# Performance work log

Measured on AMD Instinct MI355X. Metric: run time of the kernel, lower is better.

Reference implementation:

```python
import jax, jax.numpy as jnp
import numpy as np

B = 64            # number of graphs
N = 2048          # nodes per graph (equal segments; torch.stack in the original requires this)
D = 256           # hidden_dim
G = 4             # num_groups
SUBS = 3          # subclasses per group -> num_classes = 12
C = G * SUBS


def _layer_norm(x, g, b, eps=1e-5):
    mu = jnp.mean(x, axis=-1, keepdims=True)
    var = jnp.var(x, axis=-1, keepdims=True)
    return (x - mu) * jax.lax.rsqrt(var + eps) * g + b


def setup_inputs() -> dict:
    key = jax.random.key(0)
    ks = jax.random.split(key, 20)
    T = B * N
    inp = {
        "node_features": jax.random.normal(ks[0], (T, D), dtype=jnp.float32),
        "batch": jnp.repeat(jnp.arange(B, dtype=jnp.int64), N),  # sorted, equal-size segments
        # group queries (nn.Parameter randn)
        "group_queries": jax.random.normal(ks[1], (G, D), dtype=jnp.float32),
        # per-group projector MLP: D -> 2D -> SUBS*D (stacked over groups)
        "proj_w1": jax.random.normal(ks[2], (G, D, 2 * D), dtype=jnp.float32) * (1.0 / np.sqrt(D)),
        "proj_b1": jnp.zeros((G, 2 * D), dtype=jnp.float32),
        "proj_w2": jax.random.normal(ks[3], (G, 2 * D, SUBS * D), dtype=jnp.float32) * (1.0 / np.sqrt(2 * D)),
        "proj_b2": jnp.zeros((G, SUBS * D), dtype=jnp.float32),
        # output_proj_12: LN -> Linear(D, D//2) -> ReLU -> Linear(D//2, 1)
        "ln12_g": jnp.ones((D,), dtype=jnp.float32),
        "ln12_b": jnp.zeros((D,), dtype=jnp.float32),
        "w12a": jax.random.normal(ks[4], (D, D // 2), dtype=jnp.float32) * (1.0 / np.sqrt(D)),
        "b12a": jnp.zeros((D // 2,), dtype=jnp.float32),
        "w12b": jax.random.normal(ks[5], (D // 2, 1), dtype=jnp.float32) * (1.0 / np.sqrt(D // 2)),
        "b12b": jnp.zeros((1,), dtype=jnp.float32),
        # output_proj_4
        "ln4_g": jnp.ones((D,), dtype=jnp.float32),
        "ln4_b": jnp.zeros((D,), dtype=jnp.float32),
        "w4a": jax.random.normal(ks[6], (D, D // 2), dtype=jnp.float32) * (1.0 / np.sqrt(D)),
        "b4a": jnp.zeros((D // 2,), dtype=jnp.float32),
        "w4b": jax.random.normal(ks[7], (D // 2, 1), dtype=jnp.float32) * (1.0 / np.sqrt(D // 2)),
        "b4b": jnp.zeros((1,), dtype=jnp.float32),
    }
    return inp


def reference(node_features, batch, group_queries, proj_w1, proj_b1, proj_w2, proj_b2,
              ln12_g, ln12_b, w12a, b12a, w12b, b12b,
              ln4_g, ln4_b, w4a, b4a, w4b, b4b):
    # --- derive class queries from group queries (per-group MLP) ---
    h = jax.nn.relu(jnp.einsum('gd,gdh->gh', group_queries, proj_w1) + proj_b1)   # [G, 2D]
    flat = jnp.einsum('gh,ghk->gk', h, proj_w2) + proj_b2                         # [G, SUBS*D]
    # group g maps to global class indices [3g, 3g+1, 3g+2] -> simple reshape gives ordered queries
    class_queries = flat.reshape(C, D)                                            # [12, D]

    scale = jnp.asarray(D ** 0.5, node_features.dtype)
    # equal-size sorted segments: reshape total nodes into [B, N, D] per-graph blocks
    nodes = node_features.reshape(B, N, D)

    # --- 12-class attention pooling ---
    scores12 = jnp.einsum('cd,bnd->bcn', class_queries, nodes) / scale            # [B, 12, N]
    attn12 = jax.nn.softmax(scores12, axis=-1)
    pooled12 = jnp.einsum('bcn,bnd->bcd', attn12, nodes)                          # [B, 12, D]
    x12 = _layer_norm(pooled12, ln12_g, ln12_b)
    logits_12 = (jax.nn.relu(x12 @ w12a + b12a) @ w12b + b12b)[..., 0]            # [B, 12]

    # --- 4-group attention pooling ---
    scores4 = jnp.einsum('gd,bnd->bgn', group_queries, nodes) / scale             # [B, 4, N]
    attn4 = jax.nn.softmax(scores4, axis=-1)
    pooled4 = jnp.einsum('bgn,bnd->bgd', attn4, nodes)                            # [B, 4, D]
    x4 = _layer_norm(pooled4, ln4_g, ln4_b)
    logits_4 = (jax.nn.relu(x4 @ w4a + b4a) @ w4b + b4b)[..., 0]                  # [B, 4]

    return (logits_12, logits_4, attn12)
```

## Files before the change

### kernel.cpp

```cpp
#include <hip/hip_runtime.h>
#include <math.h>

#define BG   64
#define NN   2048
#define DD   256
#define CQ   16
#define CS   128
#define NCH  16

static constexpr size_t WS_Q16 = 0;
static constexpr size_t WS_H   = 4096;
static constexpr size_t WS_S   = 6144;
static constexpr size_t WS_ML  = WS_S + (size_t)BG * 12 * NN;
static constexpr size_t WS_PL  = WS_ML + (size_t)BG * NCH * 32;

__global__ __launch_bounds__(256) void kA1(const float* __restrict__ gq,
                                           const float* __restrict__ w1,
                                           const float* __restrict__ b1,
                                           float* __restrict__ ws) {
    int blk = blockIdx.x;
    int g   = blk >> 4;
    int jb  = (blk & 15) * 32;
    int t   = threadIdx.x;
    __shared__ float qlds[256];
    qlds[t] = gq[g * 256 + t];
    if ((blk & 15) == 0) ws[WS_Q16 + (12 + g) * 256 + t] = gq[g * 256 + t];
    __syncthreads();
    int jl = t & 31, dp = t >> 5;
    float acc = 0.f;
    const float* wp = w1 + ((size_t)g * 256) * 512 + jb + jl;
    #pragma unroll 8
    for (int i = 0; i < 32; ++i) {
        int d = dp * 32 + i;
        acc += qlds[d] * wp[(size_t)d * 512];
    }
    __shared__ float red[8][33];
    red[dp][jl] = acc;
    __syncthreads();
    if (dp == 0) {
        float s = 0.f;
        #pragma unroll
        for (int p = 0; p < 8; ++p) s += red[p][jl];
        s += b1[g * 512 + jb + jl];
        ws[WS_H + g * 512 + jb + jl] = fmaxf(s, 0.f);
    }
}

__global__ __launch_bounds__(256) void kA2(const float* __restrict__ w2,
                                           const float* __restrict__ b2,
                                           float* __restrict__ ws) {
    int blk = blockIdx.x;
    int g   = blk / 48;
    int kb  = (blk % 48) * 16;
    int t   = threadIdx.x;
    __shared__ float hlds[512];
    hlds[t]       = ws[WS_H + g * 512 + t];
    hlds[t + 256] = ws[WS_H + g * 512 + t + 256];
    __syncthreads();
    int kl = t & 15, dp = t >> 4;
    float acc = 0.f;
    const float* wp = w2 + ((size_t)g * 512) * 768 + kb + kl;
    #pragma unroll 8
    for (int i = 0; i < 32; ++i) {
        int jj = dp * 32 + i;
        acc += hlds[jj] * wp[(size_t)jj * 768];
    }
    __shared__ float red[16][17];
    red[dp][kl] = acc;
    __syncthreads();
    if (dp == 0) {
        float s = 0.f;
        #pragma unroll
        for (int p = 0; p < 16; ++p) s += red[p][kl];
        ws[WS_Q16 + g * 768 + kb + kl] = s + b2[g * 768 + kb + kl];
    }
}

__global__ __launch_bounds__(256, 4) void kF(const float* __restrict__ x,
                                             float* __restrict__ ws) {
    __shared__ float4 qlds[CQ * 64];
    __shared__ float  wlds[CQ * CS];
    __shared__ float  mbuf[CQ], lbuf[CQ];

    int t   = threadIdx.x;
    int blk = blockIdx.x;
    int b   = blk >> 4, ch = blk & 15;
    int gn0 = b * NN + ch * CS;

    const float4* qg = (const float4*)(ws + WS_Q16);
    #pragma unroll
    for (int i = 0; i < 4; ++i) qlds[t + i * 256] = qg[t + i * 256];
    __syncthreads();

    int node = t & 127, half = t >> 7;
    const float4* xa = (const float4*)x + (size_t)(gn0 + node) * 64 + half * 32;
    float sc[CQ];
    #pragma unroll
    for (int c = 0; c < CQ; ++c) sc[c] = 0.f;

    float4 buf[8];
    #pragma unroll
    for (int i = 0; i < 8; ++i) buf[i] = xa[i];
    for (int base = 0; base < 32; base += 8) {
        float4 cur[8];
        #pragma unroll
        for (int i = 0; i < 8; ++i) cur[i] = buf[i];
        if (base + 8 < 32) {
            #pragma unroll
            for (int i = 0; i < 8; ++i) buf[i] = xa[base + 8 + i];
        }
        #pragma unroll
        for (int i = 0; i < 8; ++i) {
            #pragma unroll
            for (int c = 0; c < CQ; ++c) {
                float4 q = qlds[c * 64 + half * 32 + base + i];
                sc[c] += q.x * cur[i].x + q.y * cur[i].y
                       + q.z * cur[i].z + q.w * cur[i].w;
            }
        }
    }

    if (half == 1) {
        #pragma unroll
        for (int c = 0; c < CQ; ++c) wlds[c * CS + node] = sc[c];
    }
    __syncthreads();
    if (half == 0) {
        #pragma unroll
        for (int c = 0; c < CQ; ++c)
            wlds[c * CS + node] = (sc[c] + wlds[c * CS + node]) * 0.0625f;
    }
    __syncthreads();

    {
        float* srow = ws + WS_S + (size_t)b * 12 * NN + ch * CS;
        #pragma unroll
        for (int k = 0; k < 6; ++k) {
            int idx = k * 256 + t;
            srow[(size_t)(idx >> 7) * NN + (idx & 127)] = wlds[idx];
        }
    }

    {
        int c = t >> 4, slot = t & 15;
        float mv = -1e30f;
        #pragma unroll
        for (int k = 0; k < 8; ++k) mv = fmaxf(mv, wlds[c * CS + slot + k * 16]);
        #pragma unroll
        for (int off = 1; off < 16; off <<= 1) mv = fmaxf(mv, __shfl_xor(mv, off, 64));
        if (slot == 0) mbuf[c] = mv;
    }
    __syncthreads();
    #pragma unroll
    for (int k = 0; k < 8; ++k) {
        int idx = k * 256 + t;
        wlds[idx] = __expf(wlds[idx] - mbuf[idx >> 7]);
    }
    __syncthreads();
    {
        int c = t >> 4, slot = t & 15;
        float lv = 0.f;
        #pragma unroll
        for (int k = 0; k < 8; ++k) lv += wlds[c * CS + slot + k * 16];
        #pragma unroll
        for (int off = 1; off < 16; off <<= 1) lv += __shfl_xor(lv, off, 64);
        if (slot == 0) lbuf[c] = lv;
    }
    __syncthreads();
    if (t < CQ) {
        ws[WS_ML + (size_t)blk * 32 + t]      = mbuf[t];
        ws[WS_ML + (size_t)blk * 32 + 16 + t] = lbuf[t];
    }

    int wave = t >> 6, lane = t & 63;
    int ng = wave & 1, cg = wave >> 1;
    float4 acc[8];
    #pragma unroll
    for (int j = 0; j < 8; ++j) acc[j] = make_float4(0.f, 0.f, 0.f, 0.f);

    const float4* xq = (const float4*)x + (size_t)(gn0 + ng * 64) * 64 + lane;
    for (int nq = 0; nq < 16; ++nq) {
        float4 x0 = xq[(size_t)(nq * 4 + 0) * 64];
        float4 x1 = xq[(size_t)(nq * 4 + 1) * 64];
        float4 x2 = xq[(size_t)(nq * 4 + 2) * 64];
        float4 x3 = xq[(size_t)(nq * 4 + 3) * 64];
        #pragma unroll
        for (int j = 0; j < 8; ++j) {
            int c = cg * 8 + j;
            float4 ev = *(const float4*)&wlds[c * CS + ng * 64 + nq * 4];
            acc[j].x += ev.x * x0.x + ev.y * x1.x + ev.z * x2.x + ev.w * x3.x;
            acc[j].y += ev.x * x0.y + ev.y * x1.y + ev.z * x2.y + ev.w * x3.y;
            acc[j].z += ev.x * x0.z + ev.y * x1.z + ev.z * x2.z + ev.w * x3.z;
            acc[j].w += ev.x * x0.w + ev.y * x1.w + ev.z * x2.w + ev.w * x3.w;
        }
    }

    float4* sdata = qlds;
    if (ng == 0) {
        #pragma unroll
        for (int j = 0; j < 8; ++j) sdata[(cg * 8 + j) * 64 + lane] = acc[j];
    }
    __syncthreads();
    if (ng == 1) {
        #pragma unroll
        for (int j = 0; j < 8; ++j) {
            float4* p = &sdata[(cg * 8 + j) * 64 + lane];
            float4 v = *p;
            v.x += acc[j].x; v.y += acc[j].y; v.z += acc[j].z; v.w += acc[j].w;
            *p = v;
        }
    }
    __syncthreads();
    float* po = ws + WS_PL + (size_t)blk * (CQ * 256);
    const float* sf = (const float*)sdata;
    #pragma unroll
    for (int i = 0; i < CQ; ++i) po[t + i * 256] = sf[t + i * 256];
}

__global__ __launch_bounds__(256) void kE(float* __restrict__ ws,
        const float* __restrict__ lnG12, const float* __restrict__ lnB12,
        const float* __restrict__ wA12,  const float* __restrict__ bA12,
        const float* __restrict__ wB12,  const float* __restrict__ bB12,
        const float* __restrict__ lnG4,  const float* __restrict__ lnB4,
        const float* __restrict__ wA4,   const float* __restrict__ bA4,
        const float* __restrict__ wB4,   const float* __restrict__ bB4,
        float* __restrict__ out) {
    int bc = blockIdx.x;
    int b = bc >> 4, c = bc & 15;
    int t = threadIdx.x, wave = t >> 6, lane = t & 63;

    __shared__ float scl[NCH];
    __shared__ float sinvl, smv;
    if (t < NCH) {
        float mi = ws[WS_ML + (size_t)(b * NCH + t) * 32 + c];
        float li = ws[WS_ML + (size_t)(b * NCH + t) * 32 + 16 + c];
        float m = mi;
        #pragma unroll
        for (int off = 1; off < 16; off <<= 1) m = fmaxf(m, __shfl_xor(m, off, 64));
        float e = __expf(mi - m);
        float pl = e * li;
        #pragma unroll
        for (int off = 1; off < 16; off <<= 1) pl += __shfl_xor(pl, off, 64);
        scl[t] = e;
        if (t == 0) {
            sinvl = 1.f / pl;
            smv   = m;
        }
    }
    __syncthreads();

    float v = 0.f;
    for (int i = 0; i < NCH; ++i)
        v += scl[i] * ws[WS_PL + ((size_t)(b * NCH + i) * CQ + c) * 256 + t];
    v *= sinvl;

    if (c < 12) {
        float m  = smv;
        float il = sinvl;
        const float4* sr = (const float4*)(ws + WS_S + ((size_t)b * 12 + c) * NN);
        float4* ar = (float4*)(out + 1024) + ((size_t)b * 12 + c) * (NN / 4);
        #pragma unroll
        for (int k = 0; k < 2; ++k) {
            float4 s4 = sr[t + k * 256];
            float4 e4;
            e4.x = __expf(s4.x - m) * il;
            e4.y = __expf(s4.y - m) * il;
            e4.z = __expf(s4.z - m) * il;
            e4.w = __expf(s4.w - m) * il;
            ar[t + k * 256] = e4;
        }
    }

    __shared__ float wr1[4], wr2[4];
    float s = v;
    #pragma unroll
    for (int off = 32; off; off >>= 1) s += __shfl_xor(s, off, 64);
    if (lane == 0) wr1[wave] = s;
    __syncthreads();
    float mu = (wr1[0] + wr1[1] + wr1[2] + wr1[3]) * (1.f / 256.f);
    float dv = v - mu;
    s = dv * dv;
    #pragma unroll
    for (int off = 32; off; off >>= 1) s += __shfl_xor(s, off, 64);
    if (lane == 0) wr2[wave] = s;
    __syncthreads();
    float var = (wr2[0] + wr2[1] + wr2[2] + wr2[3]) * (1.f / 256.f);

    bool is12 = (c < 12);
    const float* lg = is12 ? lnG12 : lnG4;
    const float* lb = is12 ? lnB12 : lnB4;
    const float* wA = is12 ? wA12  : wA4;
    const float* bA = is12 ? bA12  : bA4;
    const float* wB = is12 ? wB12  : wB4;
    const float* bB = is12 ? bB12  : bB4;

    __shared__ float ylds[256];
    __shared__ float hred[256];
    __shared__ float hlds[128];
    float y = dv * rsqrtf(var + 1e-5f) * lg[t] + lb[t];
    ylds[t] = y;
    __syncthreads();
    {
        int j = t & 127, half = t >> 7;
        float hh = 0.f;
        const float* wc = wA + (size_t)half * 128 * 128 + j;
        #pragma unroll 4
        for (int d = 0; d < 128; ++d) hh += ylds[half * 128 + d] * wc[(size_t)d * 128];
        hred[t] = hh;
    }
    __syncthreads();
    if (t < 128) hlds[t] = fmaxf(hred[t] + hred[t + 128] + bA[t], 0.f);
    __syncthreads();
    if (t < 64) {
        float pp = hlds[t] * wB[t] + hlds[t + 64] * wB[t + 64];
        #pragma unroll
        for (int off = 32; off; off >>= 1) pp += __shfl_xor(pp, off, 64);
        if (t == 0) {
            float logit = pp + bB[0];
            if (is12) out[b * 12 + c] = logit;
            else      out[768 + b * 4 + (c - 12)] = logit;
        }
    }
}

extern "C" void kernel_launch(void* const* d_in, const int* in_sizes, int n_in,
                              void* d_out, int out_size, void* d_ws, size_t ws_size,
                              hipStream_t stream) {
    const float* x     = (const float*)d_in[0];
    const float* gq    = (const float*)d_in[2];
    const float* w1    = (const float*)d_in[3];
    const float* b1    = (const float*)d_in[4];
    const float* w2    = (const float*)d_in[5];
    const float* b2    = (const float*)d_in[6];
    const float* ln12g = (const float*)d_in[7];
    const float* ln12b = (const float*)d_in[8];
    const float* w12a  = (const float*)d_in[9];
    const float* b12a  = (const float*)d_in[10];
    const float* w12b  = (const float*)d_in[11];
    const float* b12b  = (const float*)d_in[12];
    const float* ln4g  = (const float*)d_in[13];
    const float* ln4b  = (const float*)d_in[14];
    const float* w4a   = (const float*)d_in[15];
    const float* b4a   = (const float*)d_in[16];
    const float* w4b   = (const float*)d_in[17];
    const float* b4b   = (const float*)d_in[18];

    float* out = (float*)d_out;
    float* ws  = (float*)d_ws;

    kA1<<<64,       256, 0, stream>>>(gq, w1, b1, ws);
    kA2<<<192,      256, 0, stream>>>(w2, b2, ws);
    kF <<<BG * NCH, 256, 0, stream>>>(x, ws);
    kE <<<1024,     256, 0, stream>>>(ws,
            ln12g, ln12b, w12a, b12a, w12b, b12b,
            ln4g,  ln4b,  w4a,  b4a,  w4b,  b4b, out);
}
```

Baseline: 280.4 us.

## Split fused pooling kernel across query halves to double block count

The fused score/softmax/pooling kernel now launches two blocks per 128-node chunk, each handling 8 of the 16 queries. This halves registers and LDS per block and raises the occupancy hint to 8. It also drops the cross-wave reduction in the pooling stage, so each wave now covers all 128 nodes for two queries. The cost is that each node chunk is read from global memory twice, once per query half.

```diff
diff --git a/kernel.cpp b/kernel.cpp
--- a/kernel.cpp
+++ b/kernel.cpp
@@ -76,27 +76,29 @@
     }
 }
 
-__global__ __launch_bounds__(256, 4) void kF(const float* __restrict__ x,
+__global__ __launch_bounds__(256, 8) void kF(const float* __restrict__ x,
                                              float* __restrict__ ws) {
-    __shared__ float4 qlds[CQ * 64];
-    __shared__ float  wlds[CQ * CS];
-    __shared__ float  mbuf[CQ], lbuf[CQ];
-
-    int t   = threadIdx.x;
-    int blk = blockIdx.x;
-    int b   = blk >> 4, ch = blk & 15;
-    int gn0 = b * NN + ch * CS;
-
-    const float4* qg = (const float4*)(ws + WS_Q16);
-    #pragma unroll
-    for (int i = 0; i < 4; ++i) qlds[t + i * 256] = qg[t + i * 256];
+    __shared__ float4 qlds[8 * 64];
+    __shared__ float  wlds[8 * CS];
+    __shared__ float  mbuf[8];
+
+    int t     = threadIdx.x;
+    int blk   = blockIdx.x;
+    int chalf = blk & 1;
+    int ch    = (blk >> 1) & 15;
+    int b     = blk >> 5;
+    int gn0   = b * NN + ch * CS;
+
+    const float4* qg = (const float4*)(ws + WS_Q16) + (size_t)chalf * 8 * 64;
+    qlds[t]       = qg[t];
+    qlds[t + 256] = qg[t + 256];
     __syncthreads();
 
     int node = t & 127, half = t >> 7;
     const float4* xa = (const float4*)x + (size_t)(gn0 + node) * 64 + half * 32;
-    float sc[CQ];
-    #pragma unroll
-    for (int c = 0; c < CQ; ++c) sc[c] = 0.f;
+    float sc[8];
+    #pragma unroll
+    for (int c = 0; c < 8; ++c) sc[c] = 0.f;
 
     float4 buf[8];
     #pragma unroll
@@ -112,7 +114,7 @@
         #pragma unroll
         for (int i = 0; i < 8; ++i) {
             #pragma unroll
-            for (int c = 0; c < CQ; ++c) {
+            for (int c = 0; c < 8; ++c) {
                 float4 q = qlds[c * 64 + half * 32 + base + i];
                 sc[c] += q.x * cur[i].x + q.y * cur[i].y
                        + q.z * cur[i].z + q.w * cur[i].w;
@@ -122,12 +124,12 @@
 
     if (half == 1) {
         #pragma unroll
-        for (int c = 0; c < CQ; ++c) wlds[c * CS + node] = sc[c];
+        for (int c = 0; c < 8; ++c) wlds[c * CS + node] = sc[c];
     }
     __syncthreads();
     if (half == 0) {
         #pragma unroll
-        for (int c = 0; c < CQ; ++c)
+        for (int c = 0; c < 8; ++c)
             wlds[c * CS + node] = (sc[c] + wlds[c * CS + node]) * 0.0625f;
     }
     __syncthreads();
@@ -135,86 +137,70 @@
     {
         float* srow = ws + WS_S + (size_t)b * 12 * NN + ch * CS;
         #pragma unroll
-        for (int k = 0; k < 6; ++k) {
+        for (int k = 0; k < 4; ++k) {
             int idx = k * 256 + t;
-            srow[(size_t)(idx >> 7) * NN + (idx & 127)] = wlds[idx];
+            int cl  = idx >> 7, nn = idx & 127;
+            int gc  = chalf * 8 + cl;
+            if (gc < 12) srow[(size_t)gc * NN + nn] = wlds[idx];
         }
     }
 
     {
-        int c = t >> 4, slot = t & 15;
+        int cl = t >> 5, slot = t & 31;
         float mv = -1e30f;
         #pragma unroll
-        for (int k = 0; k < 8; ++k) mv = fmaxf(mv, wlds[c * CS + slot + k * 16]);
-        #pragma unroll
-        for (int off = 1; off < 16; off <<= 1) mv = fmaxf(mv, __shfl_xor(mv, off, 64));
-        if (slot == 0) mbuf[c] = mv;
-    }
-    __syncthreads();
-    #pragma unroll
-    for (int k = 0; k < 8; ++k) {
+        for (int k = 0; k < 4; ++k) mv = fmaxf(mv, wlds[cl * CS + slot + k * 32]);
+        #pragma unroll
+        for (int off = 1; off < 32; off <<= 1) mv = fmaxf(mv, __shfl_xor(mv, off, 64));
+        if (slot == 0) mbuf[cl] = mv;
+    }
+    __syncthreads();
+    #pragma unroll
+    for (int k = 0; k < 4; ++k) {
         int idx = k * 256 + t;
         wlds[idx] = __expf(wlds[idx] - mbuf[idx >> 7]);
     }
     __syncthreads();
     {
-        int c = t >> 4, slot = t & 15;
+        int cl = t >> 5, slot = t & 31;
         float lv = 0.f;
         #pragma unroll
-        for (int k = 0; k < 8; ++k) lv += wlds[c * CS + slot + k * 16];
-        #pragma unroll
-        for (int off = 1; off < 16; off <<= 1) lv += __shfl_xor(lv, off, 64);
-        if (slot == 0) lbuf[c] = lv;
-    }
-    __syncthreads();
-    if (t < CQ) {
-        ws[WS_ML + (size_t)blk * 32 + t]      = mbuf[t];
-        ws[WS_ML + (size_t)blk * 32 + 16 + t] = lbuf[t];
+        for (int k = 0; k < 4; ++k) lv += wlds[cl * CS + slot + k * 32];
+        #pragma unroll
+        for (int off = 1; off < 32; off <<= 1) lv += __shfl_xor(lv, off, 64);
+        if (slot == 0) {
+            size_t mlb = WS_ML + (size_t)(b * NCH + ch) * 32 + chalf * 8 + cl;
+            ws[mlb]      = mbuf[cl];
+            ws[mlb + 16] = lv;
+        }
     }
 
     int wave = t >> 6, lane = t & 63;
-    int ng = wave & 1, cg = wave >> 1;
-    float4 acc[8];
-    #pragma unroll
-    for (int j = 0; j < 8; ++j) acc[j] = make_float4(0.f, 0.f, 0.f, 0.f);
-
-    const float4* xq = (const float4*)x + (size_t)(gn0 + ng * 64) * 64 + lane;
-    for (int nq = 0; nq < 16; ++nq) {
+    float4 acc0 = make_float4(0.f, 0.f, 0.f, 0.f);
+    float4 acc1 = make_float4(0.f, 0.f, 0.f, 0.f);
+    int c0 = wave * 2;
+
+    const float4* xq = (const float4*)x + (size_t)gn0 * 64 + lane;
+    for (int nq = 0; nq < 32; ++nq) {
         float4 x0 = xq[(size_t)(nq * 4 + 0) * 64];
         float4 x1 = xq[(size_t)(nq * 4 + 1) * 64];
         float4 x2 = xq[(size_t)(nq * 4 + 2) * 64];
         float4 x3 = xq[(size_t)(nq * 4 + 3) * 64];
-        #pragma unroll
-        for (int j = 0; j < 8; ++j) {
-            int c = cg * 8 + j;
-            float4 ev = *(const float4*)&wlds[c * CS + ng * 64 + nq * 4];
-            acc[j].x += ev.x * x0.x + ev.y * x1.x + ev.z * x2.x + ev.w * x3.x;
-            acc[j].y += ev.x * x0.y + ev.y * x1.y + ev.z * x2.y + ev.w * x3.y;
-            acc[j].z += ev.x * x0.z + ev.y * x1.z + ev.z * x2.z + ev.w * x3.z;
-            acc[j].w += ev.x * x0.w + ev.y * x1.w + ev.z * x2.w + ev.w * x3.w;
-        }
-    }
-
-    float4* sdata = qlds;
-    if (ng == 0) {
-        #pragma unroll
-        for (int j = 0; j < 8; ++j) sdata[(cg * 8 + j) * 64 + lane] = acc[j];
-    }
-    __syncthreads();
-    if (ng == 1) {
-        #pragma unroll
-        for (int j = 0; j < 8; ++j) {
-            float4* p = &sdata[(cg * 8 + j) * 64 + lane];
-            float4 v = *p;
-            v.x += acc[j].x; v.y += acc[j].y; v.z += acc[j].z; v.w += acc[j].w;
-            *p = v;
-        }
-    }
-    __syncthreads();
-    float* po = ws + WS_PL + (size_t)blk * (CQ * 256);
-    const float* sf = (const float*)sdata;
-    #pragma unroll
-    for (int i = 0; i < CQ; ++i) po[t + i * 256] = sf[t + i * 256];
+        float4 e0 = *(const float4*)&wlds[c0 * CS + nq * 4];
+        float4 e1 = *(const float4*)&wlds[(c0 + 1) * CS + nq * 4];
+        acc0.x += e0.x * x0.x + e0.y * x1.x + e0.z * x2.x + e0.w * x3.x;
+        acc0.y += e0.x * x0.y + e0.y * x1.y + e0.z * x2.y + e0.w * x3.y;
+        acc0.z += e0.x * x0.z + e0.y * x1.z + e0.z * x2.z + e0.w * x3.z;
+        acc0.w += e0.x * x0.w + e0.y * x1.w + e0.z * x2.w + e0.w * x3.w;
+        acc1.x += e1.x * x0.x + e1.y * x1.x + e1.z * x2.x + e1.w * x3.x;
+        acc1.y += e1.x * x0.y + e1.y * x1.y + e1.z * x2.y + e1.w * x3.y;
+        acc1.z += e1.x * x0.z + e1.y * x1.z + e1.z * x2.z + e1.w * x3.z;
+        acc1.w += e1.x * x0.w + e1.y * x1.w + e1.z * x2.w + e1.w * x3.w;
+    }
+
+    float4* po = (float4*)(ws + WS_PL + (size_t)(b * NCH + ch) * (CQ * 256));
+    po[(chalf * 8 + c0) * 64 + lane]     = acc0;
+    po[(chalf * 8 + c0 + 1) * 64 + lane] = acc1;
 }
 
 __global__ __launch_bounds__(256) void kE(float* __restrict__ ws,
@@ -348,10 +334,10 @@
     float* out = (float*)d_out;
     float* ws  = (float*)d_ws;
 
-    kA1<<<64,       256, 0, stream>>>(gq, w1, b1, ws);
-    kA2<<<192,      256, 0, stream>>>(w2, b2, ws);
-    kF <<<BG * NCH, 256, 0, stream>>>(x, ws);
-    kE <<<1024,     256, 0, stream>>>(ws,
+    kA1<<<64,         256, 0, stream>>>(gq, w1, b1, ws);
+    kA2<<<192,        256, 0, stream>>>(w2, b2, ws);
+    kF <<<BG*NCH*2,   256, 0, stream>>>(x, ws);
+    kE <<<1024,       256, 0, stream>>>(ws,
             ln12g, ln12b, w12a, b12a, w12b, b12b,
             ln4g,  ln4b,  w4a,  b4a,  w4b,  b4b, out);
 }
```

After: 566.3 us. 2.02x slower.

## Halve kF chunk size, split score dot over waves, read queries from global

Applied to the files above, without the earlier changes.

The fused score/softmax/pool kernel now handles 64-node chunks (32 chunks per graph) instead of 128. Each wave computes a quarter of the D dimension for all 16 queries, reading the queries straight from global memory with wave-uniform addresses instead of staging them in LDS. Partial scores are reduced through LDS, and each wave then pools 4 queries over all 64 nodes, which removes the cross-wave accumulator reduction. The goal is more blocks and higher occupancy with less LDS, at the cost of twice as many partial rows for the final combine kernel to merge.

```diff
diff --git a/kernel.cpp b/kernel.cpp
--- a/kernel.cpp
+++ b/kernel.cpp
@@ -5,8 +5,8 @@
 #define NN   2048
 #define DD   256
 #define CQ   16
-#define CS   128
-#define NCH  16
+#define CS   64
+#define NCH  32
 
 static constexpr size_t WS_Q16 = 0;
 static constexpr size_t WS_H   = 4096;
@@ -76,118 +76,98 @@
     }
 }
 
-__global__ __launch_bounds__(256, 4) void kF(const float* __restrict__ x,
+__global__ __launch_bounds__(256, 6) void kF(const float* __restrict__ x,
+                                             const float* __restrict__ q16,
                                              float* __restrict__ ws) {
-    __shared__ float4 qlds[CQ * 64];
-    __shared__ float  wlds[CQ * CS];
-    __shared__ float  mbuf[CQ], lbuf[CQ];
-
-    int t   = threadIdx.x;
-    int blk = blockIdx.x;
-    int b   = blk >> 4, ch = blk & 15;
-    int gn0 = b * NN + ch * CS;
-
-    const float4* qg = (const float4*)(ws + WS_Q16);
-    #pragma unroll
-    for (int i = 0; i < 4; ++i) qlds[t + i * 256] = qg[t + i * 256];
-    __syncthreads();
-
-    int node = t & 127, half = t >> 7;
-    const float4* xa = (const float4*)x + (size_t)(gn0 + node) * 64 + half * 32;
-    float sc[CQ];
-    #pragma unroll
-    for (int c = 0; c < CQ; ++c) sc[c] = 0.f;
-
-    float4 buf[8];
-    #pragma unroll
-    for (int i = 0; i < 8; ++i) buf[i] = xa[i];
-    for (int base = 0; base < 32; base += 8) {
-        float4 cur[8];
-        #pragma unroll
-        for (int i = 0; i < 8; ++i) cur[i] = buf[i];
-        if (base + 8 < 32) {
-            #pragma unroll
-            for (int i = 0; i < 8; ++i) buf[i] = xa[base + 8 + i];
-        }
-        #pragma unroll
-        for (int i = 0; i < 8; ++i) {
-            #pragma unroll
-            for (int c = 0; c < CQ; ++c) {
-                float4 q = qlds[c * 64 + half * 32 + base + i];
-                sc[c] += q.x * cur[i].x + q.y * cur[i].y
-                       + q.z * cur[i].z + q.w * cur[i].w;
-            }
-        }
-    }
-
-    if (half == 1) {
-        #pragma unroll
-        for (int c = 0; c < CQ; ++c) wlds[c * CS + node] = sc[c];
-    }
-    __syncthreads();
-    if (half == 0) {
-        #pragma unroll
-        for (int c = 0; c < CQ; ++c)
-            wlds[c * CS + node] = (sc[c] + wlds[c * CS + node]) * 0.0625f;
-    }
+    __shared__ float red[4 * 16 * 64];
+    __shared__ float mbuf[16];
+
+    int t    = threadIdx.x;
+    int blk  = blockIdx.x;
+    int b    = blk >> 5, ch = blk & 31;
+    int gn0  = b * NN + ch * CS;
+
+    int lane = t & 63;
+    int wave = t >> 6;
+    int qoff = __builtin_amdgcn_readfirstlane(wave * 64);
+
+    const float4* xa = (const float4*)x + (size_t)(gn0 + lane) * 64 + wave * 16;
+    const float*  qb = q16 + qoff;
+    float sc[16];
+    #pragma unroll
+    for (int c = 0; c < 16; ++c) sc[c] = 0.f;
+
+    #pragma unroll 4
+    for (int i = 0; i < 16; ++i) {
+        float4 xi = xa[i];
+        #pragma unroll
+        for (int c = 0; c < 16; ++c) {
+            float4 q4 = *(const float4*)(qb + c * 256 + i * 4);
+            sc[c] += q4.x * xi.x + q4.y * xi.y + q4.z * xi.z + q4.w * xi.w;
+        }
+    }
+
+    #pragma unroll
+    for (int c = 0; c < 16; ++c) red[wave * 1024 + c * 64 + lane] = sc[c];
     __syncthreads();
 
     {
         float* srow = ws + WS_S + (size_t)b * 12 * NN + ch * CS;
         #pragma unroll
-        for (int k = 0; k < 6; ++k) {
-            int idx = k * 256 + t;
-            srow[(size_t)(idx >> 7) * NN + (idx & 127)] = wlds[idx];
-        }
-    }
+        for (int k = 0; k < 4; ++k) {
+            int o = k * 256 + t;
+            float s = (red[o] + red[o + 1024] + red[o + 2048] + red[o + 3072])
+                      * 0.0625f;
+            red[o] = s;
+            int c = o >> 6;
+            if (c < 12) srow[(size_t)c * NN + (o & 63)] = s;
+        }
+    }
+    __syncthreads();
 
     {
         int c = t >> 4, slot = t & 15;
         float mv = -1e30f;
         #pragma unroll
-        for (int k = 0; k < 8; ++k) mv = fmaxf(mv, wlds[c * CS + slot + k * 16]);
+        for (int k = 0; k < 4; ++k) mv = fmaxf(mv, red[c * 64 + slot + k * 16]);
         #pragma unroll
         for (int off = 1; off < 16; off <<= 1) mv = fmaxf(mv, __shfl_xor(mv, off, 64));
-        if (slot == 0) mbuf[c] = mv;
-    }
-    __syncthreads();
-    #pragma unroll
-    for (int k = 0; k < 8; ++k) {
-        int idx = k * 256 + t;
-        wlds[idx] = __expf(wlds[idx] - mbuf[idx >> 7]);
+        if (slot == 0) {
+            mbuf[c] = mv;
+            ws[WS_ML + (size_t)blk * 32 + c] = mv;
+        }
+    }
+    __syncthreads();
+    #pragma unroll
+    for (int k = 0; k < 4; ++k) {
+        int o = k * 256 + t;
+        red[o] = __expf(red[o] - mbuf[o >> 6]);
     }
     __syncthreads();
     {
         int c = t >> 4, slot = t & 15;
         float lv = 0.f;
         #pragma unroll
-        for (int k = 0; k < 8; ++k) lv += wlds[c * CS + slot + k * 16];
+        for (int k = 0; k < 4; ++k) lv += red[c * 64 + slot + k * 16];
         #pragma unroll
         for (int off = 1; off < 16; off <<= 1) lv += __shfl_xor(lv, off, 64);
-        if (slot == 0) lbuf[c] = lv;
-    }
-    __syncthreads();
-    if (t < CQ) {
-        ws[WS_ML + (size_t)blk * 32 + t]      = mbuf[t];
-        ws[WS_ML + (size_t)blk * 32 + 16 + t] = lbuf[t];
-    }
-
-    int wave = t >> 6, lane = t & 63;
-    int ng = wave & 1, cg = wave >> 1;
-    float4 acc[8];
-    #pragma unroll
-    for (int j = 0; j < 8; ++j) acc[j] = make_float4(0.f, 0.f, 0.f, 0.f);
-
-    const float4* xq = (const float4*)x + (size_t)(gn0 + ng * 64) * 64 + lane;
+        if (slot == 0) ws[WS_ML + (size_t)blk * 32 + 16 + c] = lv;
+    }
+
+    int c0 = wave * 4;
+    float4 acc[4];
+    #pragma unroll
+    for (int j = 0; j < 4; ++j) acc[j] = make_float4(0.f, 0.f, 0.f, 0.f);
+
+    const float4* xq = (const float4*)x + (size_t)gn0 * 64 + lane;
     for (int nq = 0; nq < 16; ++nq) {
         float4 x0 = xq[(size_t)(nq * 4 + 0) * 64];
         float4 x1 = xq[(size_t)(nq * 4 + 1) * 64];
         float4 x2 = xq[(size_t)(nq * 4 + 2) * 64];
         float4 x3 = xq[(size_t)(nq * 4 + 3) * 64];
         #pragma unroll
-        for (int j = 0; j < 8; ++j) {
-            int c = cg * 8 + j;
-            float4 ev = *(const float4*)&wlds[c * CS + ng * 64 + nq * 4];
+        for (int j = 0; j < 4; ++j) {
+            float4 ev = *(const float4*)&red[(c0 + j) * 64 + nq * 4];
             acc[j].x += ev.x * x0.x + ev.y * x1.x + ev.z * x2.x + ev.w * x3.x;
             acc[j].y += ev.x * x0.y + ev.y * x1.y + ev.z * x2.y + ev.w * x3.y;
             acc[j].z += ev.x * x0.z + ev.y * x1.z + ev.z * x2.z + ev.w * x3.z;
@@ -195,26 +175,9 @@
         }
     }
 
-    float4* sdata = qlds;
-    if (ng == 0) {
-        #pragma unroll
-        for (int j = 0; j < 8; ++j) sdata[(cg * 8 + j) * 64 + lane] = acc[j];
-    }
-    __syncthreads();
-    if (ng == 1) {
-        #pragma unroll
-        for (int j = 0; j < 8; ++j) {
-            float4* p = &sdata[(cg * 8 + j) * 64 + lane];
-            float4 v = *p;
-            v.x += acc[j].x; v.y += acc[j].y; v.z += acc[j].z; v.w += acc[j].w;
-            *p = v;
-        }
-    }
-    __syncthreads();
-    float* po = ws + WS_PL + (size_t)blk * (CQ * 256);
-    const float* sf = (const float*)sdata;
-    #pragma unroll
-    for (int i = 0; i < CQ; ++i) po[t + i * 256] = sf[t + i * 256];
+    float4* po = (float4*)(ws + WS_PL + (size_t)blk * (CQ * 256));
+    #pragma unroll
+    for (int j = 0; j < 4; ++j) po[(c0 + j) * 64 + lane] = acc[j];
 }
 
 __global__ __launch_bounds__(256) void kE(float* __restrict__ ws,
@@ -236,11 +199,11 @@
         float li = ws[WS_ML + (size_t)(b * NCH + t) * 32 + 16 + c];
         float m = mi;
         #pragma unroll
-        for (int off = 1; off < 16; off <<= 1) m = fmaxf(m, __shfl_xor(m, off, 64));
+        for (int off = 1; off < 32; off <<= 1) m = fmaxf(m, __shfl_xor(m, off, 64));
         float e = __expf(mi - m);
         float pl = e * li;
         #pragma unroll
-        for (int off = 1; off < 16; off <<= 1) pl += __shfl_xor(pl, off, 64);
+        for (int off = 1; off < 32; off <<= 1) pl += __shfl_xor(pl, off, 64);
         scl[t] = e;
         if (t == 0) {
             sinvl = 1.f / pl;
@@ -350,7 +313,7 @@
 
     kA1<<<64,       256, 0, stream>>>(gq, w1, b1, ws);
     kA2<<<192,      256, 0, stream>>>(w2, b2, ws);
-    kF <<<BG * NCH, 256, 0, stream>>>(x, ws);
+    kF <<<BG * NCH, 256, 0, stream>>>(x, ws + WS_Q16, ws);
     kE <<<1024,     256, 0, stream>>>(ws,
             ln12g, ln12b, w12a, b12a, w12b, b12b,
             ln4g,  ln4b,  w4a,  b4a,  w4b,  b4b, out);
```

Measured after the change: 593.0 us. 2.11x slower.
